# Kernel tuning notes

Measured on AMD Instinct MI355X. Metric: run time of the kernel, lower is better.

## Reference

```python
import jax, jax.numpy as jnp
import numpy as np


def furthest_point_sample(points, n_samples):
    """Iterative farthest point sampling.
    points: [B, M, 3] float. Returns idx [B, n_samples] int32.
    Matches the CUDA kernel semantics: first selected index is 0, then
    greedily pick the point maximizing min squared distance to selected set.
    """
    B, M, _ = points.shape

    def step(carry, _):
        min_d, last = carry                       # [B, M], [B]
        p = jnp.take_along_axis(points, last[:, None, None], axis=1)  # [B,1,3]
        d = jnp.sum((points - p) ** 2, axis=-1)   # [B, M]
        min_d = jnp.minimum(min_d, d)
        nxt = jnp.argmax(min_d, axis=1).astype(jnp.int32)
        return (min_d, nxt), last

    init = (jnp.full((B, M), jnp.finfo(points.dtype).max, points.dtype),
            jnp.zeros((B,), jnp.int32))
    _, idxs = jax.lax.scan(step, init, None, length=n_samples)  # [S, B]
    return idxs.T  # [B, S]


def gather_points(feats, idx):
    """feats: [B, C, M], idx: [B, S] -> [B, C, S]"""
    return jnp.take_along_axis(feats, idx[:, None, :], axis=2)


def setup_inputs() -> dict:
    key = jax.random.key(0)
    k1, k2 = jax.random.split(key)
    B, Np, Nc = 128, 16384, 4096
    partial = jax.random.normal(k1, (B, Np, 3), dtype=jnp.float32)
    coarse = jax.random.normal(k2, (B, 3, Nc), dtype=jnp.float32)
    return {"partial": partial, "coarse": coarse, "merge_points": 2048}


def reference(partial, coarse, merge_points):
    # Model.forward core: partial -> [B,3,N], merge with coarse, FPS + gather
    partial_t = jnp.transpose(partial, (0, 2, 1))            # [B, 3, Np]
    coarse_merge = jnp.concatenate([partial_t, coarse], axis=2)  # [B, 3, M]
    pts = jnp.transpose(coarse_merge, (0, 2, 1))             # [B, M, 3]
    idx = furthest_point_sample(pts, merge_points)           # [B, S]
    return gather_points(coarse_merge, idx)                  # [B, 3, S]
```

## Files before the change

kernel.cpp:

```cpp
#include <hip/hip_runtime.h>
#include <cfloat>

#define BATCH 128
#define NP    16384
#define NC    4096
#define MPTS  (NP + NC)
#define SOUT  2048
#define NTHR  1024
#define KPT   20

#define DPP_MAX_STEP(ctrl, rmask)                                                  \
    {                                                                              \
        unsigned int lo2 = (unsigned int)__builtin_amdgcn_update_dpp(              \
            0, (int)klo, (ctrl), (rmask), 0xF, false);                             \
        unsigned int hi2 = (unsigned int)__builtin_amdgcn_update_dpp(              \
            0, (int)khi, (ctrl), (rmask), 0xF, false);                             \
        const unsigned long long a =                                               \
            ((unsigned long long)khi << 32) | (unsigned long long)klo;             \
        const unsigned long long c =                                               \
            ((unsigned long long)hi2 << 32) | (unsigned long long)lo2;             \
        if (c > a) { klo = lo2; khi = hi2; }                                       \
    }

__global__ __launch_bounds__(NTHR)
__attribute__((amdgpu_waves_per_eu(4, 4)))
void fps_kernel(
    const float* __restrict__ partial,
    const float* __restrict__ coarse,
    float* __restrict__ out)
{
    const int b = blockIdx.x;
    const int t = threadIdx.x;
    const int lane = t & 63;

    __shared__ float s_q[4];
    __shared__ unsigned long long s_key[2];

    float x[KPT], y[KPT], z[KPT], md[KPT];

    const float* Pb = partial + (size_t)b * NP * 3;
    const float* Cb = coarse + (size_t)b * 3 * NC;

#pragma unroll
    for (int k = 0; k < KPT; ++k) {
        const int m = k * NTHR + t;
        if (k < 16) {
            x[k] = Pb[m * 3 + 0];
            y[k] = Pb[m * 3 + 1];
            z[k] = Pb[m * 3 + 2];
        } else {
            const int j = m - NP;
            x[k] = Cb[0 * NC + j];
            y[k] = Cb[1 * NC + j];
            z[k] = Cb[2 * NC + j];
        }
        md[k] = FLT_MAX;
    }

    float* outb = out + (size_t)b * 3 * SOUT;

    if (t == 0) {
        s_q[0] = x[0]; s_q[1] = y[0]; s_q[2] = z[0];
        outb[0 * SOUT + 0] = x[0];
        outb[1 * SOUT + 0] = y[0];
        outb[2 * SOUT + 0] = z[0];
        s_key[0] = 0ULL; s_key[1] = 0ULL;
    }
    __syncthreads();

    float qx = s_q[0], qy = s_q[1], qz = s_q[2];

    for (int s = 0; s < SOUT - 1; ++s) {
        const int cur = s & 1, nxt = cur ^ 1;

        float bv = -1.0f;
        int bi = 0;
#pragma unroll
        for (int k = 0; k < KPT; ++k) {
            const float dx = __fsub_rn(x[k], qx);
            const float dy = __fsub_rn(y[k], qy);
            const float dz = __fsub_rn(z[k], qz);
            const float dy2 = __fmul_rn(dy, dy);
            const float d = __builtin_fmaf(dz, dz, __builtin_fmaf(dx, dx, dy2));
            const float nmd = fminf(md[k], d);
            md[k] = nmd;
            if (nmd > bv) { bv = nmd; bi = k; }
        }

        unsigned int klo = ~((unsigned int)((bi << 10) | t));
        unsigned int khi = __float_as_uint(bv);

        DPP_MAX_STEP(0x111, 0xF)
        DPP_MAX_STEP(0x112, 0xF)
        DPP_MAX_STEP(0x114, 0xF)
        DPP_MAX_STEP(0x118, 0xF)
        DPP_MAX_STEP(0x142, 0xa)
        DPP_MAX_STEP(0x143, 0xc)

        if (lane == 63) {
            atomicMax(&s_key[cur],
                      ((unsigned long long)khi << 32) | (unsigned long long)klo);
        }
        if (t == 0) s_key[nxt] = 0ULL;
        __syncthreads();

        const unsigned long long wk = s_key[cur];
        const unsigned int mid = ~((unsigned int)(wk & 0xFFFFFFFFULL));
        if ((mid & (NTHR - 1)) == (unsigned int)t) {
            const int kk = (int)(mid >> 10);
            float wx = 0.f, wy = 0.f, wz = 0.f;
#pragma unroll
            for (int k = 0; k < KPT; ++k) {
                if (k == kk) { wx = x[k]; wy = y[k]; wz = z[k]; }
            }
            s_q[0] = wx; s_q[1] = wy; s_q[2] = wz;
            const int slot = s + 1;
            outb[0 * SOUT + slot] = wx;
            outb[1 * SOUT + slot] = wy;
            outb[2 * SOUT + slot] = wz;
        }
        __syncthreads();

        qx = s_q[0]; qy = s_q[1]; qz = s_q[2];
    }
}

extern "C" void kernel_launch(void* const* d_in, const int* in_sizes, int n_in,
                              void* d_out, int out_size, void* d_ws, size_t ws_size,
                              hipStream_t stream) {
    (void)in_sizes; (void)n_in; (void)d_ws; (void)ws_size; (void)out_size;
    const float* partial = (const float*)d_in[0];
    const float* coarse  = (const float*)d_in[1];
    float* out = (float*)d_out;
    fps_kernel<<<dim3(BATCH), dim3(NTHR), 0, stream>>>(partial, coarse, out);
}
```

Baseline: 3.464 ms.

## Shrink block to 256 threads and fetch FPS winner coordinates from global memory

Cuts each block from 16 waves to 4, with 80 points held in registers per thread. The per-step reduction becomes one barrier: each wave writes its DPP-reduced key to its own LDS slot, and every thread takes the max of the 4 slots. All threads then reload the winning point's coordinates from global memory, which removes the second barrier and the shared-memory broadcast of the query point. In exchange there is a dependent global load on every iteration, one wave per SIMD to hide latency, very high register pressure, and a possible reuse race on the LDS key slots since only one barrier separates iterations.

```diff
diff --git a/kernel.cpp b/kernel.cpp
--- a/kernel.cpp
+++ b/kernel.cpp
@@ -6,8 +6,9 @@
 #define NC    4096
 #define MPTS  (NP + NC)
 #define SOUT  2048
-#define NTHR  1024
-#define KPT   20
+#define NTHR  256
+#define KPT   80
+#define KPART 64
 
 #define DPP_MAX_STEP(ctrl, rmask)                                                  \
     {                                                                              \
@@ -23,7 +24,7 @@
     }
 
 __global__ __launch_bounds__(NTHR)
-__attribute__((amdgpu_waves_per_eu(4, 4)))
+__attribute__((amdgpu_waves_per_eu(1, 1)))
 void fps_kernel(
     const float* __restrict__ partial,
     const float* __restrict__ coarse,
@@ -31,10 +32,10 @@
 {
     const int b = blockIdx.x;
     const int t = threadIdx.x;
+    const int wid = t >> 6;
     const int lane = t & 63;
 
-    __shared__ float s_q[4];
-    __shared__ unsigned long long s_key[2];
+    __shared__ unsigned long long s_keys[4];
 
     float x[KPT], y[KPT], z[KPT], md[KPT];
 
@@ -44,7 +45,7 @@
 #pragma unroll
     for (int k = 0; k < KPT; ++k) {
         const int m = k * NTHR + t;
-        if (k < 16) {
+        if (k < KPART) {
             x[k] = Pb[m * 3 + 0];
             y[k] = Pb[m * 3 + 1];
             z[k] = Pb[m * 3 + 2];
@@ -59,20 +60,14 @@
 
     float* outb = out + (size_t)b * 3 * SOUT;
 
+    float qx = Pb[0], qy = Pb[1], qz = Pb[2];
     if (t == 0) {
-        s_q[0] = x[0]; s_q[1] = y[0]; s_q[2] = z[0];
-        outb[0 * SOUT + 0] = x[0];
-        outb[1 * SOUT + 0] = y[0];
-        outb[2 * SOUT + 0] = z[0];
-        s_key[0] = 0ULL; s_key[1] = 0ULL;
+        outb[0 * SOUT + 0] = qx;
+        outb[1 * SOUT + 0] = qy;
+        outb[2 * SOUT + 0] = qz;
     }
-    __syncthreads();
-
-    float qx = s_q[0], qy = s_q[1], qz = s_q[2];
 
     for (int s = 0; s < SOUT - 1; ++s) {
-        const int cur = s & 1, nxt = cur ^ 1;
-
         float bv = -1.0f;
         int bi = 0;
 #pragma unroll
@@ -87,7 +82,7 @@
             if (nmd > bv) { bv = nmd; bi = k; }
         }
 
-        unsigned int klo = ~((unsigned int)((bi << 10) | t));
+        unsigned int klo = ~((unsigned int)((bi << 8) | t));
         unsigned int khi = __float_as_uint(bv);
 
         DPP_MAX_STEP(0x111, 0xF)
@@ -98,30 +93,31 @@
         DPP_MAX_STEP(0x143, 0xc)
 
         if (lane == 63) {
-            atomicMax(&s_key[cur],
-                      ((unsigned long long)khi << 32) | (unsigned long long)klo);
-        }
-        if (t == 0) s_key[nxt] = 0ULL;
-        __syncthreads();
-
-        const unsigned long long wk = s_key[cur];
-        const unsigned int mid = ~((unsigned int)(wk & 0xFFFFFFFFULL));
-        if ((mid & (NTHR - 1)) == (unsigned int)t) {
-            const int kk = (int)(mid >> 10);
-            float wx = 0.f, wy = 0.f, wz = 0.f;
-#pragma unroll
-            for (int k = 0; k < KPT; ++k) {
-                if (k == kk) { wx = x[k]; wy = y[k]; wz = z[k]; }
-            }
-            s_q[0] = wx; s_q[1] = wy; s_q[2] = wz;
-            const int slot = s + 1;
-            outb[0 * SOUT + slot] = wx;
-            outb[1 * SOUT + slot] = wy;
-            outb[2 * SOUT + slot] = wz;
+            s_keys[wid] = ((unsigned long long)khi << 32) | (unsigned long long)klo;
         }
         __syncthreads();
 
-        qx = s_q[0]; qy = s_q[1]; qz = s_q[2];
+        unsigned long long wk = s_keys[0];
+        const unsigned long long k1 = s_keys[1];
+        const unsigned long long k2 = s_keys[2];
+        const unsigned long long k3 = s_keys[3];
+        if (k1 > wk) wk = k1;
+        if (k2 > wk) wk = k2;
+        if (k3 > wk) wk = k3;
+        const unsigned int m = ~((unsigned int)wk);
+
+        const int j = (int)m - NP;
+        const float* ax = (m < NP) ? (Pb + (size_t)m * 3 + 0) : (Cb + 0 * NC + j);
+        const float* ay = (m < NP) ? (Pb + (size_t)m * 3 + 1) : (Cb + 1 * NC + j);
+        const float* az = (m < NP) ? (Pb + (size_t)m * 3 + 2) : (Cb + 2 * NC + j);
+        qx = *ax; qy = *ay; qz = *az;
+
+        if (t == 0) {
+            const int slot = s + 1;
+            outb[0 * SOUT + slot] = qx;
+            outb[1 * SOUT + slot] = qy;
+            outb[2 * SOUT + slot] = qz;
+        }
     }
 }
 
```

Result: slower. 5.261 ms (+51.9%).
